# Kernel tuning notes

Measured on AMD Instinct MI355X. Metric: run time of the kernel, lower is better.

## Reference

```python
import jax, jax.numpy as jnp
import numpy as np

N = 100000
E = 3200000
IN_DIM, HID_DIM, OUT_DIM = 29, 64, 2


def setup_inputs() -> dict:
    key = jax.random.key(0)
    k1, k2, k3, k4, k5 = jax.random.split(key, 5)
    x = jax.random.normal(k1, (N, IN_DIM), dtype=jnp.float32)
    edge_index = jax.random.randint(k2, (2, E), 0, N, dtype=jnp.int64)
    # GCNConv params: glorot-ish weights, zero bias (bias added after aggregation)
    W1 = jax.random.normal(k3, (IN_DIM, HID_DIM), dtype=jnp.float32) * (1.0 / np.sqrt(IN_DIM))
    b1 = jnp.zeros((HID_DIM,), dtype=jnp.float32)
    W2 = jax.random.normal(k4, (HID_DIM, OUT_DIM), dtype=jnp.float32) * (1.0 / np.sqrt(HID_DIM))
    b2 = jnp.zeros((OUT_DIM,), dtype=jnp.float32)
    return {"x": x, "edge_index": edge_index, "W1": W1, "b1": b1, "W2": W2, "b2": b2}


def _gcn_norm(edge_index, n_nodes):
    # PyG gcn_norm with add_self_loops=True, symmetric D^-1/2 A D^-1/2
    loop = jnp.arange(n_nodes, dtype=edge_index.dtype)
    src = jnp.concatenate([edge_index[0], loop])
    dst = jnp.concatenate([edge_index[1], loop])
    deg = jax.ops.segment_sum(jnp.ones_like(dst, dtype=jnp.float32), dst, num_segments=n_nodes)
    dinv = jnp.where(deg > 0, jax.lax.rsqrt(deg), 0.0)
    norm = dinv[src] * dinv[dst]  # [E + N]
    return src, dst, norm


def _gcn_conv(x, src, dst, norm, W, b):
    h = x @ W                      # [N, d_out] -- transform first (smaller msgs)
    msg = h[src] * norm[:, None]   # [E+N, d_out] gather + scale
    out = jax.ops.segment_sum(msg, dst, num_segments=x.shape[0])  # scatter-add
    return out + b


def reference(x, edge_index, W1, b1, W2, b2):
    src, dst, norm = _gcn_norm(edge_index, x.shape[0])
    h = _gcn_conv(x, src, dst, norm, W1, b1)
    h = jax.nn.relu(h)
    out = _gcn_conv(h, src, dst, norm, W2, b2)
    return out
```

## Files before the change

kernel.cpp:

```cpp
#include <hip/hip_runtime.h>

#define N_NODES 100000
#define N_EDGES 3200000
#define IN_DIM  29
#define HID_DIM 64
#define NBUCK   391
#define BNODES  256
#define CAP     10496
#define PEPT    16
#define PEPB    16384
#define PSTAGE  22272

#define OFF_CUR   0
#define OFF_ROWS  512
#define OFF_ROWE  100512
#define OFF_DINV  200512
#define OFF_ZS    300512
#define OFF_EBUF  500544
#define OFF_XS    4604480

static __device__ __forceinline__ unsigned short f2bf(float f) {
    unsigned u = __float_as_uint(f);
    u += 0x7fffu + ((u >> 16) & 1u);
    return (unsigned short)(u >> 16);
}

static __device__ __forceinline__ void unpack_add(float4& acc, uint2 a) {
    acc.x += __uint_as_float(a.x << 16);
    acc.y += __uint_as_float(a.x & 0xFFFF0000u);
    acc.z += __uint_as_float(a.y << 16);
    acc.w += __uint_as_float(a.y & 0xFFFF0000u);
}

__global__ __launch_bounds__(1024) void partition_kernel(const int* __restrict__ ei,
        int* __restrict__ gcursor, int* __restrict__ ebuf) {
    __shared__ int lhist[NBUCK];
    __shared__ int lcur[NBUCK];
    __shared__ int gbase[NBUCK];
    __shared__ int soff[NBUCK];
    __shared__ int sc[NBUCK];
    __shared__ int stage[PSTAGE];
    int tid = threadIdx.x;
    for (int i = tid; i < NBUCK; i += 1024) lhist[i] = 0;
    __syncthreads();

    int base = blockIdx.x * PEPB + tid * PEPT;
    bool valid = (base < N_EDGES);
    if (valid) {
        const int4* dp = (const int4*)(ei + N_EDGES + base);
        #pragma unroll
        for (int q = 0; q < 4; ++q) {
            int4 t = dp[q];
            atomicAdd(&lhist[t.x >> 8], 1); atomicAdd(&lhist[t.y >> 8], 1);
            atomicAdd(&lhist[t.z >> 8], 1); atomicAdd(&lhist[t.w >> 8], 1);
        }
    }
    __syncthreads();
    int c = 0, p = 0;
    if (tid < NBUCK) { c = lhist[tid]; p = (c + 15) & ~15; sc[tid] = p; }
    __syncthreads();
    for (int off = 1; off < NBUCK; off <<= 1) {
        int t = 0;
        if (tid < NBUCK && tid >= off) t = sc[tid - off];
        __syncthreads();
        if (tid < NBUCK) sc[tid] += t;
        __syncthreads();
    }
    if (tid < NBUCK) {
        int so = sc[tid] - p;
        soff[tid] = so;
        lcur[tid] = so;
        gbase[tid] = p ? (tid * CAP + atomicAdd(&gcursor[tid], p)) : 0;
    }
    __syncthreads();
    if (valid) {
        const int4* dp = (const int4*)(ei + N_EDGES + base);
        const int4* sp = (const int4*)(ei + base);
        #pragma unroll
        for (int q = 0; q < 4; ++q) {
            int4 d = dp[q];
            int4 s = sp[q];
            int pos;
            pos = atomicAdd(&lcur[d.x >> 8], 1); stage[pos] = s.x | ((d.x & 255) << 17);
            pos = atomicAdd(&lcur[d.y >> 8], 1); stage[pos] = s.y | ((d.y & 255) << 17);
            pos = atomicAdd(&lcur[d.z >> 8], 1); stage[pos] = s.z | ((d.z & 255) << 17);
            pos = atomicAdd(&lcur[d.w >> 8], 1); stage[pos] = s.w | ((d.w & 255) << 17);
        }
    }
    __syncthreads();
    if (tid < NBUCK) {
        int endReal = lcur[tid];
        int endPad  = soff[tid] + (((lhist[tid]) + 15) & ~15);
        for (int k = endReal; k < endPad; ++k) stage[k] = -1;
    }
    __syncthreads();
    int wv = tid >> 6, ln = tid & 63;
    for (int b = wv; b < NBUCK; b += 16) {
        int np = (lhist[b] + 15) & ~15;
        int so = soff[b], gb = gbase[b];
        for (int k = ln; k < np; k += 64)
            ebuf[gb + k] = stage[so + k];
    }
}

__global__ __launch_bounds__(1024) void bucketsort_kernel(const int* __restrict__ gcursor,
        int* __restrict__ ebuf, int* __restrict__ rowStart, int* __restrict__ rowEnd,
        float* __restrict__ dinv, float* __restrict__ zs) {
    __shared__ int cnt[BNODES];
    __shared__ int cur[BNODES];
    __shared__ int stage[CAP];
    int b = blockIdx.x, tid = threadIdx.x;
    if (tid < BNODES) cnt[tid] = 0;
    __syncthreads();
    int base = b * CAP;
    int size = gcursor[b];

    for (int j = tid; j < size; j += 1024) {
        unsigned p = (unsigned)ebuf[base + j];
        stage[j] = (int)p;
        if (p != 0xFFFFFFFFu) atomicAdd(&cnt[p >> 17], 1);
    }
    __syncthreads();

    int v = 0, vp = 0;
    if (tid < BNODES) { v = cnt[tid]; vp = (v + 7) & ~7; cur[tid] = vp; }
    __syncthreads();
    for (int off = 1; off < BNODES; off <<= 1) {
        int t = 0;
        if (tid < BNODES && tid >= off) t = cur[tid - off];
        __syncthreads();
        if (tid < BNODES) cur[tid] += t;
        __syncthreads();
    }
    if (tid < BNODES) {
        int excl = cur[tid] - vp;
        int node = b * BNODES + tid;
        if (node < N_NODES) {
            rowStart[node] = base + excl;
            rowEnd[node]   = base + excl + vp;
            dinv[node]     = rsqrtf((float)v + 1.0f);
            for (int p2 = excl + v; p2 < excl + vp; ++p2)
                ebuf[base + p2] = N_NODES;
        }
        cur[tid] = excl;
    }
    __syncthreads();
    for (int j = tid; j < size; j += 1024) {
        unsigned p = (unsigned)stage[j];
        if (p != 0xFFFFFFFFu) {
            int pos = atomicAdd(&cur[p >> 17], 1);
            ebuf[base + pos] = (int)(p & 0x1FFFF);
        }
    }
    if (b == 0 && tid == 0) {
        zs[2 * N_NODES]     = 0.0f;
        zs[2 * N_NODES + 1] = 0.0f;
    }
}

__global__ __launch_bounds__(256) void xs_kernel(const float* __restrict__ x,
        const float* __restrict__ dinv, unsigned int* __restrict__ xsb) {
    int i = blockIdx.x * 256 + threadIdx.x;
    if (i >= (N_NODES + 1) * 16) return;
    int nd = i >> 4, kp = i & 15;
    unsigned u = 0u;
    if (nd < N_NODES) {
        float dn = dinv[nd];
        int k0 = kp * 2, k1 = k0 + 1;
        float f0 = (k0 < IN_DIM) ? x[nd * IN_DIM + k0] * dn : 0.0f;
        float f1 = (k1 < IN_DIM) ? x[nd * IN_DIM + k1] * dn : 0.0f;
        u = (unsigned)f2bf(f0) | ((unsigned)f2bf(f1) << 16);
    }
    xsb[i] = u;
}

#define XROW(i) (((unsigned)(i) << 6) | moff)

#define PREP(P, rs, re, node)                                            \
    int P##i0, P##i1, P##i2, P##i3, P##i4, P##i5;                        \
    {                                                                    \
        int relim = max((re) - 1, (rs));                                 \
        int j0 = (rs) + q;                                               \
        int t0 = ebuf[min(j0,      relim)];                              \
        int t1 = ebuf[min(j0 + 8,  relim)];                              \
        int t2 = ebuf[min(j0 + 16, relim)];                              \
        int t3 = ebuf[min(j0 + 24, relim)];                              \
        int t4 = ebuf[min(j0 + 32, relim)];                              \
        P##i0 = (j0      < (re)) ? t0 : N_NODES;                         \
        P##i1 = (j0 + 8  < (re)) ? t1 : N_NODES;                         \
        P##i2 = (j0 + 16 < (re)) ? t2 : N_NODES;                         \
        P##i3 = (j0 + 24 < (re)) ? t3 : N_NODES;                         \
        P##i4 = (j0 + 32 < (re)) ? t4 : N_NODES;                         \
        P##i5 = (q == 0) ? (node) : N_NODES;    \
    }

#define GATH(G, P)                                                       \
    uint2 G##0 = *(const uint2*)(xb + XROW(P##i0));                      \
    uint2 G##1 = *(const uint2*)(xb + XROW(P##i1));                      \
    uint2 G##2 = *(const uint2*)(xb + XROW(P##i2));                      \
    uint2 G##3 = *(const uint2*)(xb + XROW(P##i3));                      \
    uint2 G##4 = *(const uint2*)(xb + XROW(P##i4));                      \
    uint2 G##5 = *(const uint2*)(xb + XROW(P##i5));

#define UNP(acc, G)                                                      \
    unpack_add(acc, G##0); unpack_add(acc, G##1); unpack_add(acc, G##2); \
    unpack_add(acc, G##3); unpack_add(acc, G##4); unpack_add(acc, G##5);

#define TAIL(acc, rs, re)                                                \
    {                                                                    \
        int j = (rs) + q + 40;                                           \
        while (j < (re)) {                  \
            int s = ebuf[j];                                             \
            uint2 a = *(const uint2*)(xb + XROW(s));                     \
            unpack_add(acc, a);                                          \
            j += 8;                                                      \
        }                                                                \
    }

static __device__ __forceinline__ void mlp2_store(float4 aA, float4 aB,
        int nodeA, int nodeB, int lane,
        const float* w1s, const float* b1s, const float* w2s,
        const float* __restrict__ dinv, float* __restrict__ zs) {
    #pragma unroll
    for (int msk = 8; msk <= 32; msk <<= 1) {
        aA.x += __shfl_xor(aA.x, msk); aB.x += __shfl_xor(aB.x, msk);
        aA.y += __shfl_xor(aA.y, msk); aB.y += __shfl_xor(aB.y, msk);
        aA.z += __shfl_xor(aA.z, msk); aB.z += __shfl_xor(aB.z, msk);
        aA.w += __shfl_xor(aA.w, msk); aB.w += __shfl_xor(aB.w, msk);
    }
    float dnA = dinv[nodeA], dnB = dinv[nodeB];
    aA.x *= dnA; aA.y *= dnA; aA.z *= dnA; aA.w *= dnA;
    aB.x *= dnB; aB.y *= dnB; aB.z *= dnB; aB.w *= dnB;

    float hA = b1s[lane], hB = b1s[lane];
    #pragma unroll
    for (int kk = 0; kk < IN_DIM; ++kk) {
        float w = w1s[kk * HID_DIM + lane];
        float cA = ((kk & 3) == 0) ? aA.x : ((kk & 3) == 1) ? aA.y
                 : ((kk & 3) == 2) ? aA.z : aA.w;
        float cB = ((kk & 3) == 0) ? aB.x : ((kk & 3) == 1) ? aB.y
                 : ((kk & 3) == 2) ? aB.z : aB.w;
        hA = fmaf(__shfl(cA, kk >> 2), w, hA);
        hB = fmaf(__shfl(cB, kk >> 2), w, hB);
    }
    hA = fmaxf(hA, 0.0f); hB = fmaxf(hB, 0.0f);

    float zA0 = hA * w2s[lane * 2 + 0], zA1 = hA * w2s[lane * 2 + 1];
    float zB0 = hB * w2s[lane * 2 + 0], zB1 = hB * w2s[lane * 2 + 1];
    #pragma unroll
    for (int off = 32; off > 0; off >>= 1) {
        zA0 += __shfl_down(zA0, off); zA1 += __shfl_down(zA1, off);
        zB0 += __shfl_down(zB0, off); zB1 += __shfl_down(zB1, off);
    }
    if (lane == 0) {
        float2 oA; oA.x = zA0 * dnA; oA.y = zA1 * dnA;
        float2 oB; oB.x = zB0 * dnB; oB.y = zB1 * dnB;
        *(float2*)(zs + nodeA * 2) = oA;
        *(float2*)(zs + nodeB * 2) = oB;
    }
}

__global__ __launch_bounds__(512) void fused_kernel(const unsigned int* __restrict__ xs_,
        const int* __restrict__ rowStart, const int* __restrict__ rowEnd,
        const int* __restrict__ ebuf, const float* __restrict__ dinv,
        const float* __restrict__ W1, const float* __restrict__ b1,
        const float* __restrict__ W2, float* __restrict__ zs) {
    __shared__ float w1s[IN_DIM * HID_DIM];
    __shared__ float b1s[HID_DIM];
    __shared__ float w2s[HID_DIM * 2];
    const int tid = threadIdx.x;
    for (int i = tid; i < IN_DIM * HID_DIM; i += 512) w1s[i] = W1[i];
    if (tid < HID_DIM) {
        b1s[tid] = b1[tid];
        w2s[tid * 2 + 0] = W2[tid * 2 + 0];
        w2s[tid * 2 + 1] = W2[tid * 2 + 1];
    }
    __syncthreads();

    const int lane = tid & 63;
    const int q = lane >> 3, m = lane & 7;
    const unsigned moff = (unsigned)(m << 3);
    const char* xb = (const char*)xs_;
    const int n0 = blockIdx.x * 32 + (tid >> 6) * 4;

    const int rs0 = rowStart[n0+0], re0 = rowEnd[n0+0];
    const int rs1 = rowStart[n0+1], re1 = rowEnd[n0+1];
    const int rs2 = rowStart[n0+2], re2 = rowEnd[n0+2];
    const int rs3 = rowStart[n0+3], re3 = rowEnd[n0+3];

    PREP(pa, rs0, re0, n0+0)
    PREP(pb, rs1, re1, n0+1)
    GATH(ga, pa)
    GATH(gb, pb)
    PREP(pc, rs2, re2, n0+2)
    PREP(pd, rs3, re3, n0+3)
    float4 acc0 = make_float4(0.f, 0.f, 0.f, 0.f);
    float4 acc1 = make_float4(0.f, 0.f, 0.f, 0.f);
    UNP(acc0, ga)
    TAIL(acc0, rs0, re0)
    UNP(acc1, gb)
    TAIL(acc1, rs1, re1)
    GATH(gc, pc)
    GATH(gd, pd)
    mlp2_store(acc0, acc1, n0+0, n0+1, lane, w1s, b1s, w2s, dinv, zs);

    float4 acc2 = make_float4(0.f, 0.f, 0.f, 0.f);
    float4 acc3 = make_float4(0.f, 0.f, 0.f, 0.f);
    UNP(acc2, gc)
    TAIL(acc2, rs2, re2)
    UNP(acc3, gd)
    TAIL(acc3, rs3, re3)
    mlp2_store(acc2, acc3, n0+2, n0+3, lane, w1s, b1s, w2s, dinv, zs);
}

__global__ __launch_bounds__(256) void agg2_kernel(const float* __restrict__ zs,
        const int* __restrict__ rowStart, const int* __restrict__ rowEnd,
        const int* __restrict__ ebuf, const float* __restrict__ dinv,
        const float* __restrict__ b2, float* __restrict__ out) {
    int tid = threadIdx.x;
    int node = blockIdx.x * 16 + (tid >> 4);
    if (node >= N_NODES) return;
    int gl = tid & 15;
    const float2* zs2 = (const float2*)zs;
    float a0 = 0.0f, a1 = 0.0f, c0 = 0.0f, c1 = 0.0f;
    int rs = rowStart[node], re = rowEnd[node];
    int j = rs + gl;
    for (; j + 16 < re; j += 32) {
        float2 za = zs2[ebuf[j]];
        float2 zb = zs2[ebuf[j + 16]];
        a0 += za.x; a1 += za.y;
        c0 += zb.x; c1 += zb.y;
    }
    if (j < re) {
        float2 za = zs2[ebuf[j]];
        a0 += za.x; a1 += za.y;
    }
    a0 += c0; a1 += c1;
    a0 += __shfl_xor(a0, 8); a1 += __shfl_xor(a1, 8);
    a0 += __shfl_xor(a0, 4); a1 += __shfl_xor(a1, 4);
    a0 += __shfl_xor(a0, 2); a1 += __shfl_xor(a1, 2);
    a0 += __shfl_xor(a0, 1); a1 += __shfl_xor(a1, 1);
    if (gl == 0) {
        float dn = dinv[node];
        float2 zself = zs2[node];
        float2 o;
        o.x = dn * (a0 + zself.x) + b2[0];
        o.y = dn * (a1 + zself.y) + b2[1];
        ((float2*)out)[node] = o;
    }
}

extern "C" void kernel_launch(void* const* d_in, const int* in_sizes, int n_in,
                              void* d_out, int out_size, void* d_ws, size_t ws_size,
                              hipStream_t stream) {
    const float* x  = (const float*)d_in[0];
    const int*   ei = (const int*)d_in[1];
    const float* W1 = (const float*)d_in[2];
    const float* b1 = (const float*)d_in[3];
    const float* W2 = (const float*)d_in[4];
    const float* b2 = (const float*)d_in[5];
    float* out = (float*)d_out;

    int*   wsi      = (int*)d_ws;
    float* wsf      = (float*)d_ws;
    int*   gcursor  = wsi + OFF_CUR;
    int*   rowStart = wsi + OFF_ROWS;
    int*   rowEnd   = wsi + OFF_ROWE;
    float* dinv     = wsf + OFF_DINV;
    float* zs       = wsf + OFF_ZS;
    int*   ebuf     = wsi + OFF_EBUF;
    unsigned int* xsb = (unsigned int*)(wsi + OFF_XS);

    hipMemsetAsync(gcursor, 0, NBUCK * sizeof(int), stream);
    partition_kernel<<<(N_EDGES + PEPB - 1) / PEPB, 1024, 0, stream>>>(ei, gcursor, ebuf);
    bucketsort_kernel<<<NBUCK, 1024, 0, stream>>>(gcursor, ebuf, rowStart, rowEnd, dinv, zs);
    xs_kernel<<<((N_NODES + 1) * 16 + 255) / 256, 256, 0, stream>>>(x, dinv, xsb);
    fused_kernel<<<N_NODES / 32, 512, 0, stream>>>(xsb, rowStart, rowEnd, ebuf, dinv, W1, b1, W2, zs);
    agg2_kernel<<<(N_NODES + 15) / 16, 256, 0, stream>>>(zs, rowStart, rowEnd, ebuf, dinv, b2, out);
}
```

Measured before the change: 216.2 us.

## Fuse xs conversion into bucketsort, stage sorted edges in LDS, hoist all gathers

Drops the separate xs_kernel and does the dinv-scaled bf16 conversion of x inside bucketsort, using per-block dinv kept in shared memory. Bucketsort now scatters sorted edges into LDS and writes them back to global memory coalesced, instead of doing random global scatter and padding writes. It re-reads ebuf from global on the second pass rather than staging it. The fused kernel issues all four nodes' gathers up front and adds a minimum of 4 blocks in its launch bounds. Issuing all gathers early raises register pressure, and the bucketsort blocks now do more serial work.

```diff
diff --git a/kernel.cpp b/kernel.cpp
--- a/kernel.cpp
+++ b/kernel.cpp
@@ -105,10 +105,13 @@
 
 __global__ __launch_bounds__(1024) void bucketsort_kernel(const int* __restrict__ gcursor,
         int* __restrict__ ebuf, int* __restrict__ rowStart, int* __restrict__ rowEnd,
-        float* __restrict__ dinv, float* __restrict__ zs) {
-    __shared__ int cnt[BNODES];
-    __shared__ int cur[BNODES];
-    __shared__ int stage[CAP];
+        float* __restrict__ dinv, const float* __restrict__ x,
+        unsigned int* __restrict__ xsb, float* __restrict__ zs) {
+    __shared__ int   cnt[BNODES];
+    __shared__ int   cur[BNODES];
+    __shared__ float dls[BNODES];
+    __shared__ int   stage[CAP];
+    __shared__ int   szp_sh;
     int b = blockIdx.x, tid = threadIdx.x;
     if (tid < BNODES) cnt[tid] = 0;
     __syncthreads();
@@ -117,7 +120,6 @@
 
     for (int j = tid; j < size; j += 1024) {
         unsigned p = (unsigned)ebuf[base + j];
-        stage[j] = (int)p;
         if (p != 0xFFFFFFFFu) atomicAdd(&cnt[p >> 17], 1);
     }
     __syncthreads();
@@ -138,40 +140,46 @@
         if (node < N_NODES) {
             rowStart[node] = base + excl;
             rowEnd[node]   = base + excl + vp;
-            dinv[node]     = rsqrtf((float)v + 1.0f);
-            for (int p2 = excl + v; p2 < excl + vp; ++p2)
-                ebuf[base + p2] = N_NODES;
-        }
+            float dn = rsqrtf((float)v + 1.0f);
+            dinv[node] = dn;
+            dls[tid] = dn;
+        }
+        if (tid == BNODES - 1) szp_sh = cur[tid];
         cur[tid] = excl;
-    }
-    __syncthreads();
+        for (int p2 = excl + v; p2 < excl + vp; ++p2)
+            stage[p2] = N_NODES;
+    }
+    __syncthreads();
+
     for (int j = tid; j < size; j += 1024) {
-        unsigned p = (unsigned)stage[j];
+        unsigned p = (unsigned)ebuf[base + j];
         if (p != 0xFFFFFFFFu) {
             int pos = atomicAdd(&cur[p >> 17], 1);
-            ebuf[base + pos] = (int)(p & 0x1FFFF);
+            stage[pos] = p & 0x1FFFF;
+        }
+    }
+    __syncthreads();
+    int szp = szp_sh;
+    for (int j = tid; j < szp; j += 1024)
+        ebuf[base + j] = stage[j];
+
+    for (int i = tid; i < BNODES * 16; i += 1024) {
+        int dl = i >> 4, kp = i & 15;
+        int nd = b * BNODES + dl;
+        if (nd < N_NODES) {
+            float dn = dls[dl];
+            int k0 = kp * 2, k1 = k0 + 1;
+            float f0 = (k0 < IN_DIM) ? x[nd * IN_DIM + k0] * dn : 0.0f;
+            float f1 = (k1 < IN_DIM) ? x[nd * IN_DIM + k1] * dn : 0.0f;
+            xsb[(size_t)nd * 16 + kp] = (unsigned)f2bf(f0) | ((unsigned)f2bf(f1) << 16);
+        } else if (nd == N_NODES) {
+            xsb[(size_t)nd * 16 + kp] = 0u;
         }
     }
     if (b == 0 && tid == 0) {
         zs[2 * N_NODES]     = 0.0f;
         zs[2 * N_NODES + 1] = 0.0f;
     }
-}
-
-__global__ __launch_bounds__(256) void xs_kernel(const float* __restrict__ x,
-        const float* __restrict__ dinv, unsigned int* __restrict__ xsb) {
-    int i = blockIdx.x * 256 + threadIdx.x;
-    if (i >= (N_NODES + 1) * 16) return;
-    int nd = i >> 4, kp = i & 15;
-    unsigned u = 0u;
-    if (nd < N_NODES) {
-        float dn = dinv[nd];
-        int k0 = kp * 2, k1 = k0 + 1;
-        float f0 = (k0 < IN_DIM) ? x[nd * IN_DIM + k0] * dn : 0.0f;
-        float f1 = (k1 < IN_DIM) ? x[nd * IN_DIM + k1] * dn : 0.0f;
-        u = (unsigned)f2bf(f0) | ((unsigned)f2bf(f1) << 16);
-    }
-    xsb[i] = u;
 }
 
 #define XROW(i) (((unsigned)(i) << 6) | moff)
@@ -260,7 +268,7 @@
     }
 }
 
-__global__ __launch_bounds__(512) void fused_kernel(const unsigned int* __restrict__ xs_,
+__global__ __launch_bounds__(512, 4) void fused_kernel(const unsigned int* __restrict__ xs_,
         const int* __restrict__ rowStart, const int* __restrict__ rowEnd,
         const int* __restrict__ ebuf, const float* __restrict__ dinv,
         const float* __restrict__ W1, const float* __restrict__ b1,
@@ -290,26 +298,26 @@
 
     PREP(pa, rs0, re0, n0+0)
     PREP(pb, rs1, re1, n0+1)
+    PREP(pc, rs2, re2, n0+2)
+    PREP(pd, rs3, re3, n0+3)
     GATH(ga, pa)
     GATH(gb, pb)
-    PREP(pc, rs2, re2, n0+2)
-    PREP(pd, rs3, re3, n0+3)
+    GATH(gc, pc)
+    GATH(gd, pd)
+
     float4 acc0 = make_float4(0.f, 0.f, 0.f, 0.f);
     float4 acc1 = make_float4(0.f, 0.f, 0.f, 0.f);
+    float4 acc2 = make_float4(0.f, 0.f, 0.f, 0.f);
+    float4 acc3 = make_float4(0.f, 0.f, 0.f, 0.f);
     UNP(acc0, ga)
     TAIL(acc0, rs0, re0)
     UNP(acc1, gb)
     TAIL(acc1, rs1, re1)
-    GATH(gc, pc)
-    GATH(gd, pd)
-    mlp2_store(acc0, acc1, n0+0, n0+1, lane, w1s, b1s, w2s, dinv, zs);
-
-    float4 acc2 = make_float4(0.f, 0.f, 0.f, 0.f);
-    float4 acc3 = make_float4(0.f, 0.f, 0.f, 0.f);
     UNP(acc2, gc)
     TAIL(acc2, rs2, re2)
     UNP(acc3, gd)
     TAIL(acc3, rs3, re3)
+    mlp2_store(acc0, acc1, n0+0, n0+1, lane, w1s, b1s, w2s, dinv, zs);
     mlp2_store(acc2, acc3, n0+2, n0+3, lane, w1s, b1s, w2s, dinv, zs);
 }
 
@@ -373,8 +381,7 @@
 
     hipMemsetAsync(gcursor, 0, NBUCK * sizeof(int), stream);
     partition_kernel<<<(N_EDGES + PEPB - 1) / PEPB, 1024, 0, stream>>>(ei, gcursor, ebuf);
-    bucketsort_kernel<<<NBUCK, 1024, 0, stream>>>(gcursor, ebuf, rowStart, rowEnd, dinv, zs);
-    xs_kernel<<<((N_NODES + 1) * 16 + 255) / 256, 256, 0, stream>>>(x, dinv, xsb);
+    bucketsort_kernel<<<NBUCK, 1024, 0, stream>>>(gcursor, ebuf, rowStart, rowEnd, dinv, x, xsb, zs);
     fused_kernel<<<N_NODES / 32, 512, 0, stream>>>(xsb, rowStart, rowEnd, ebuf, dinv, W1, b1, W2, zs);
     agg2_kernel<<<(N_NODES + 15) / 16, 256, 0, stream>>>(zs, rowStart, rowEnd, ebuf, dinv, b2, out);
 }
```

Result: faster. 201.5 us (-6.8%).
